# Kernel optimization log

Hardware: AMD Instinct MI355X
Metric: run time of the kernel (lower is better)

The kernel has to match this reference:

```python
import jax, jax.numpy as jnp
import numpy as np

K_SIZE = 5  # must match init_kwargs


def _local_attention(main, ref, ref_value, k_size=K_SIZE):
    """k x k windowed dot-product attention ('dot' mode of RefLocal).

    main:      [B,H,W,C] queries
    ref:       [B,H,W,C] keys (zero-padded SAME, matching extract_volume_patches)
    ref_value: [B,H,W,V] values
    Zero padding contributes logit 0 (NOT -inf), faithful to TF SAME padding.
    """
    p = (k_size - 1) // 2
    B, H, W, C = main.shape
    ref_p = jnp.pad(ref, ((0, 0), (p, p), (p, p), (0, 0)))
    val_p = jnp.pad(ref_value, ((0, 0), (p, p), (p, p), (0, 0)))

    offsets = [(i, j) for i in range(k_size) for j in range(k_size)]
    # logits[b,h,w,idx] = <main[b,h,w,:], ref shifted by offset idx>
    logits = jnp.stack(
        [jnp.einsum('bhwc,bhwc->bhw', main, ref_p[:, i:i + H, j:j + W, :])
         for (i, j) in offsets], axis=-1)  # [B,H,W,k*k]
    attn = jax.nn.softmax(logits, axis=-1)

    out = jnp.zeros(ref_value.shape, dtype=ref_value.dtype)
    for idx, (i, j) in enumerate(offsets):
        out = out + attn[..., idx][..., None] * val_p[:, i:i + H, j:j + W, :]
    return out  # [B,H,W,V]


def setup_inputs() -> dict:
    key = jax.random.key(0)
    k1, k2, k3 = jax.random.split(key, 3)
    B, H, W, C, V = 8, 96, 96, 192, 96
    return {
        'main': jax.random.normal(k1, (B, H, W, C), dtype=jnp.float32),
        'ref': jax.random.normal(k2, (B, H, W, C), dtype=jnp.float32),
        'ref_value': jax.random.normal(k3, (B, H, W, V), dtype=jnp.float32),
    }


def reference(main, ref, ref_value):
    return _local_attention(main, ref, ref_value, K_SIZE)
```

## Files before the change

kernel.cpp:

```cpp
#include <hip/hip_runtime.h>


#define BATCH 8
#define HH 96
#define WW 96
#define CH 192
#define VV 96
#define KS 5
#define PAD 2
#define TH 8
#define TW 8
#define HT (TH + 2 * PAD)
#define WT (TW + 2 * PAD)
#define NPIX (HT * WT)
#define CHUNK 32
#define SPX 32
#define BUFSZ (NPIX * SPX)
#define SSZ (2 * BUFSZ)

#define DOT4(m, k) \
  ((m).x * (k).x + (m).y * (k).y + (m).z * (k).z + (m).w * (k).w)

__device__ __forceinline__ void gload16(const float* g, float* l) {
  __builtin_amdgcn_global_load_lds(
      (const __attribute__((address_space(1))) float*)g,
      (__attribute__((address_space(3))) float*)l, 16, 0, 0);
}

__global__ __launch_bounds__(256, 2) void reflocal_kernel(
    const float* __restrict__ qry, const float* __restrict__ key,
    const float* __restrict__ val, float* __restrict__ out) {
  int braw = blockIdx.x;
  int L = (braw & 7) * 144 + (braw >> 3);
  int bb = L / 144;
  int t2 = L - bb * 144;
  int tyy = t2 / 12;
  int txx = t2 - tyy * 12;
  int h0 = tyy * TH, w0 = txx * TW;

  int tid = threadIdx.x;
  int s4 = (tid & 7) * 4;
  int pr = (tid >> 3) >> 2;
  int pc = (tid >> 3) & 3;
  int qx0 = 2 * pc;
  int wv = tid >> 6;

  __shared__ float s[SSZ];

  int pidx[5];
#pragma unroll
  for (int r = 0; r < 5; ++r) {
    int px = (tid >> 3) + 32 * r;
    if (px < NPIX) {
      int ry = px / WT, rx = px - ry * WT;
      int hh = h0 - PAD + ry, ww = w0 - PAD + rx;
      pidx[r] = ((unsigned)hh < HH && (unsigned)ww < WW)
                    ? (bb * HH + hh) * WW + ww
                    : -1;
    } else {
      pidx[r] = -2;
    }
  }

#pragma unroll
  for (int r = 0; r < 5; ++r) {
    if (pidx[r] == -1) {
      int px = (tid >> 3) + 32 * r;
      float4 z = make_float4(0.f, 0.f, 0.f, 0.f);
      *(float4*)(&s[px * SPX + s4]) = z;
      *(float4*)(&s[BUFSZ + px * SPX + s4]) = z;
    }
  }

  float lg0[25], lg1[25];
#pragma unroll
  for (int o = 0; o < 25; ++o) { lg0[o] = 0.f; lg1[o] = 0.f; }

  const float* qb0 =
      qry + (size_t)((bb * HH + h0 + pr) * WW + w0 + qx0) * CH;
  const float* qb1 = qb0 + CH;

  auto stage = [&](float* buf, const float* src, int rl, int c0) {
#pragma unroll
    for (int r = 0; r < 5; ++r) {
      int pxs = 32 * r + 8 * wv;
      if (pxs < NPIX) {
        if (pidx[r] >= 0)
          gload16(src + pidx[r] * rl + c0 + s4, buf + pxs * SPX);
      }
    }
  };

  float* const bufA = (float*)s;
  float* const bufB = (float*)s + BUFSZ;

  stage(bufA, key, CH, 0);

  float4 m0 = *(const float4*)(qb0 + s4);
  float4 m1 = *(const float4*)(qb1 + s4);

  for (int ci = 0; ci < CH / CHUNK; ++ci) {
    __syncthreads();
    float* cur = (ci & 1) ? bufB : bufA;
    float* nxt = (ci & 1) ? bufA : bufB;
    if (ci + 1 < CH / CHUNK)
      stage(nxt, key, CH, (ci + 1) * CHUNK);
    else
      stage(nxt, val, VV, 0);

    float4 mn0, mn1;
    if (ci + 1 < CH / CHUNK) {
      int cn = (ci + 1) * CHUNK + s4;
      mn0 = *(const float4*)(qb0 + cn);
      mn1 = *(const float4*)(qb1 + cn);
    }

#pragma unroll
    for (int i = 0; i < KS; ++i) {
      const float* sp = &cur[((pr + i) * WT + qx0) * SPX + s4];
      float4 kr[6];
#pragma unroll
      for (int u = 0; u < 6; ++u) kr[u] = *(const float4*)(sp + u * SPX);
#pragma unroll
      for (int j = 0; j < KS; ++j) {
        lg0[i * 5 + j] += DOT4(m0, kr[j]);
        lg1[i * 5 + j] += DOT4(m1, kr[j + 1]);
      }
    }
    m0 = mn0;
    m1 = mn1;
  }

#pragma unroll
  for (int o = 0; o < 25; ++o) {
    lg0[o] += __shfl_xor(lg0[o], 1);
    lg0[o] += __shfl_xor(lg0[o], 2);
    lg0[o] += __shfl_xor(lg0[o], 4);
    lg1[o] += __shfl_xor(lg1[o], 1);
    lg1[o] += __shfl_xor(lg1[o], 2);
    lg1[o] += __shfl_xor(lg1[o], 4);
  }

  {
    float mx = lg0[0];
#pragma unroll
    for (int o = 1; o < 25; ++o) mx = fmaxf(mx, lg0[o]);
    float sum = 0.f;
#pragma unroll
    for (int o = 0; o < 25; ++o) {
      lg0[o] = __expf(lg0[o] - mx);
      sum += lg0[o];
    }
    float inv = 1.f / sum;
#pragma unroll
    for (int o = 0; o < 25; ++o) lg0[o] *= inv;
  }
  {
    float mx = lg1[0];
#pragma unroll
    for (int o = 1; o < 25; ++o) mx = fmaxf(mx, lg1[o]);
    float sum = 0.f;
#pragma unroll
    for (int o = 0; o < 25; ++o) {
      lg1[o] = __expf(lg1[o] - mx);
      sum += lg1[o];
    }
    float inv = 1.f / sum;
#pragma unroll
    for (int o = 0; o < 25; ++o) lg1[o] *= inv;
  }

  float* ob0 = out + (size_t)((bb * HH + h0 + pr) * WW + w0 + qx0) * VV;
  float* ob1 = ob0 + VV;

  for (int vi = 0; vi < VV / CHUNK; ++vi) {
    __syncthreads();
    float* cur = (vi & 1) ? bufB : bufA;
    float* nxt = (vi & 1) ? bufA : bufB;
    if (vi + 1 < VV / CHUNK) stage(nxt, val, VV, (vi + 1) * CHUNK);

    float4 a0 = make_float4(0.f, 0.f, 0.f, 0.f);
    float4 a1 = make_float4(0.f, 0.f, 0.f, 0.f);
#pragma unroll
    for (int i = 0; i < KS; ++i) {
      const float* sp = &cur[((pr + i) * WT + qx0) * SPX + s4];
      float4 vr[6];
#pragma unroll
      for (int u = 0; u < 6; ++u) vr[u] = *(const float4*)(sp + u * SPX);
#pragma unroll
      for (int j = 0; j < KS; ++j) {
        float w0a = lg0[i * 5 + j];
        float w1a = lg1[i * 5 + j];
        a0.x += w0a * vr[j].x;     a0.y += w0a * vr[j].y;
        a0.z += w0a * vr[j].z;     a0.w += w0a * vr[j].w;
        a1.x += w1a * vr[j + 1].x; a1.y += w1a * vr[j + 1].y;
        a1.z += w1a * vr[j + 1].z; a1.w += w1a * vr[j + 1].w;
      }
    }
    int v0 = vi * CHUNK;
    *(float4*)(ob0 + v0 + s4) = a0;
    *(float4*)(ob1 + v0 + s4) = a1;
  }
}

extern "C" void kernel_launch(void* const* d_in, const int* in_sizes, int n_in,
                              void* d_out, int out_size, void* d_ws,
                              size_t ws_size, hipStream_t stream) {
  const float* qry = (const float*)d_in[0];
  const float* key = (const float*)d_in[1];
  const float* val = (const float*)d_in[2];
  float* out = (float*)d_out;

  dim3 grid(BATCH * (HH / TH) * (WW / TW));
  dim3 block(256);
  reflocal_kernel<<<grid, block, 0, stream>>>(qry, key, val, out);
}
```

Measured before the change: 178.5 us.

## Use DPP/swizzle reductions, tree softmax, deferred stores, raise occupancy hint

Replaces the shfl_xor butterfly reductions with DPP quad permutes plus a ds_swizzle, which avoids the LDS-based bpermute path. The serial max and sum chains in the softmax become balanced trees to cut dependency latency. Output stores are buffered in registers and issued after the value loop. The launch bound is raised from 2 to 4 blocks per CU, which caps registers per thread and risks spilling given the 50 logits held per thread.

```diff
diff --git a/kernel.cpp b/kernel.cpp
--- a/kernel.cpp
+++ b/kernel.cpp
@@ -17,9 +17,17 @@
 #define SPX 32
 #define BUFSZ (NPIX * SPX)
 #define SSZ (2 * BUFSZ)
+#define NVC (VV / CHUNK)
 
 #define DOT4(m, k) \
   ((m).x * (k).x + (m).y * (k).y + (m).z * (k).z + (m).w * (k).w)
+
+#define DPPADD(x, CTRL)                                              \
+  ((x) + __builtin_bit_cast(float, __builtin_amdgcn_update_dpp(      \
+             0, __builtin_bit_cast(int, (x)), (CTRL), 0xF, 0xF, true)))
+#define SWZADD(x)                                                    \
+  ((x) + __builtin_bit_cast(float, __builtin_amdgcn_ds_swizzle(      \
+             __builtin_bit_cast(int, (x)), 0x101F)))
 
 __device__ __forceinline__ void gload16(const float* g, float* l) {
   __builtin_amdgcn_global_load_lds(
@@ -27,7 +35,39 @@
       (__attribute__((address_space(3))) float*)l, 16, 0, 0);
 }
 
-__global__ __launch_bounds__(256, 2) void reflocal_kernel(
+__device__ __forceinline__ float tmax25(const float* v) {
+  float t[13];
+#pragma unroll
+  for (int i = 0; i < 12; ++i) t[i] = fmaxf(v[2 * i], v[2 * i + 1]);
+  t[12] = v[24];
+  float u[7];
+#pragma unroll
+  for (int i = 0; i < 6; ++i) u[i] = fmaxf(t[2 * i], t[2 * i + 1]);
+  u[6] = t[12];
+  float w[4];
+#pragma unroll
+  for (int i = 0; i < 3; ++i) w[i] = fmaxf(u[2 * i], u[2 * i + 1]);
+  w[3] = u[6];
+  return fmaxf(fmaxf(w[0], w[1]), fmaxf(w[2], w[3]));
+}
+
+__device__ __forceinline__ float tsum25(const float* v) {
+  float t[13];
+#pragma unroll
+  for (int i = 0; i < 12; ++i) t[i] = v[2 * i] + v[2 * i + 1];
+  t[12] = v[24];
+  float u[7];
+#pragma unroll
+  for (int i = 0; i < 6; ++i) u[i] = t[2 * i] + t[2 * i + 1];
+  u[6] = t[12];
+  float w[4];
+#pragma unroll
+  for (int i = 0; i < 3; ++i) w[i] = u[2 * i] + u[2 * i + 1];
+  w[3] = u[6];
+  return (w[0] + w[1]) + (w[2] + w[3]);
+}
+
+__global__ __launch_bounds__(256, 4) void reflocal_kernel(
     const float* __restrict__ qry, const float* __restrict__ key,
     const float* __restrict__ val, float* __restrict__ out) {
   int braw = blockIdx.x;
@@ -133,51 +173,40 @@
 
 #pragma unroll
   for (int o = 0; o < 25; ++o) {
-    lg0[o] += __shfl_xor(lg0[o], 1);
-    lg0[o] += __shfl_xor(lg0[o], 2);
-    lg0[o] += __shfl_xor(lg0[o], 4);
-    lg1[o] += __shfl_xor(lg1[o], 1);
-    lg1[o] += __shfl_xor(lg1[o], 2);
-    lg1[o] += __shfl_xor(lg1[o], 4);
+    float a = lg0[o];
+    a = DPPADD(a, 0xB1);
+    a = DPPADD(a, 0x4E);
+    lg0[o] = SWZADD(a);
+    float b = lg1[o];
+    b = DPPADD(b, 0xB1);
+    b = DPPADD(b, 0x4E);
+    lg1[o] = SWZADD(b);
   }
 
   {
-    float mx = lg0[0];
-#pragma unroll
-    for (int o = 1; o < 25; ++o) mx = fmaxf(mx, lg0[o]);
-    float sum = 0.f;
-#pragma unroll
-    for (int o = 0; o < 25; ++o) {
-      lg0[o] = __expf(lg0[o] - mx);
-      sum += lg0[o];
-    }
-    float inv = 1.f / sum;
+    float mx = tmax25(lg0);
+#pragma unroll
+    for (int o = 0; o < 25; ++o) lg0[o] = __expf(lg0[o] - mx);
+    float inv = 1.f / tsum25(lg0);
 #pragma unroll
     for (int o = 0; o < 25; ++o) lg0[o] *= inv;
   }
   {
-    float mx = lg1[0];
-#pragma unroll
-    for (int o = 1; o < 25; ++o) mx = fmaxf(mx, lg1[o]);
-    float sum = 0.f;
-#pragma unroll
-    for (int o = 0; o < 25; ++o) {
-      lg1[o] = __expf(lg1[o] - mx);
-      sum += lg1[o];
-    }
-    float inv = 1.f / sum;
+    float mx = tmax25(lg1);
+#pragma unroll
+    for (int o = 0; o < 25; ++o) lg1[o] = __expf(lg1[o] - mx);
+    float inv = 1.f / tsum25(lg1);
 #pragma unroll
     for (int o = 0; o < 25; ++o) lg1[o] *= inv;
   }
 
-  float* ob0 = out + (size_t)((bb * HH + h0 + pr) * WW + w0 + qx0) * VV;
-  float* ob1 = ob0 + VV;
-
-  for (int vi = 0; vi < VV / CHUNK; ++vi) {
+  float4 acc[NVC][2];
+#pragma unroll
+  for (int vi = 0; vi < NVC; ++vi) {
     __syncthreads();
     float* cur = (vi & 1) ? bufB : bufA;
     float* nxt = (vi & 1) ? bufA : bufB;
-    if (vi + 1 < VV / CHUNK) stage(nxt, val, VV, (vi + 1) * CHUNK);
+    if (vi + 1 < NVC) stage(nxt, val, VV, (vi + 1) * CHUNK);
 
     float4 a0 = make_float4(0.f, 0.f, 0.f, 0.f);
     float4 a1 = make_float4(0.f, 0.f, 0.f, 0.f);
@@ -197,9 +226,16 @@
         a1.z += w1a * vr[j + 1].z; a1.w += w1a * vr[j + 1].w;
       }
     }
-    int v0 = vi * CHUNK;
-    *(float4*)(ob0 + v0 + s4) = a0;
-    *(float4*)(ob1 + v0 + s4) = a1;
+    acc[vi][0] = a0;
+    acc[vi][1] = a1;
+  }
+
+  float* ob0 = out + (size_t)((bb * HH + h0 + pr) * WW + w0 + qx0) * VV;
+  float* ob1 = ob0 + VV;
+#pragma unroll
+  for (int vi = 0; vi < NVC; ++vi) {
+    *(float4*)(ob0 + vi * CHUNK + s4) = acc[vi][0];
+    *(float4*)(ob1 + vi * CHUNK + s4) = acc[vi][1];
   }
 }
 
```

After: 266.6 us. +49.3%, slower.
